# Kernel optimization log

Hardware: AMD Instinct MI355X
Metric: run time of the kernel (lower is better)

## Reference

```python
import jax, jax.numpy as jnp
import numpy as np

B, S, T, H, VS, VE = 32, 128, 128, 512, 8000, 8000


def _lstm_scan(x_proj, W_hh, bias, h0, c0):
    # x_proj: [L, B, 4H] precomputed input projections; gate order i,f,g,o (PyTorch)
    def step(carry, xp):
        h, c = carry
        gates = xp + h @ W_hh.T + bias  # [B, 4H]
        i, f, g, o = jnp.split(gates, 4, axis=-1)
        c = jax.nn.sigmoid(f) * c + jax.nn.sigmoid(i) * jnp.tanh(g)
        h = jax.nn.sigmoid(o) * jnp.tanh(c)
        return (h, c), h
    (h, c), hs = jax.lax.scan(step, (h0, c0), x_proj)
    return hs, h, c


def setup_inputs() -> dict:
    key = jax.random.key(0)
    ks = jax.random.split(key, 16)
    sc_h = 1.0 / np.sqrt(H)
    u = lambda k, shape: jax.random.uniform(k, shape, jnp.float32, -sc_h, sc_h)
    return {
        "input_batch": jax.random.randint(ks[0], (B, S), 0, VS),
        "output_batch": jax.random.randint(ks[1], (B, T), 0, VE),
        "Wa": u(ks[2], (H, H)), "ba": u(ks[3], (H,)),
        "W1": u(ks[4], (H, 2 * H)), "b1": u(ks[5], (H,)),
        "W2": u(ks[6], (VE, H)), "b2": u(ks[7], (VE,)),
        "We_ih": u(ks[8], (4 * H, VS)), "We_hh": u(ks[9], (4 * H, H)),
        "be_ih": u(ks[10], (4 * H,)), "be_hh": u(ks[11], (4 * H,)),
        "Wd_ih": u(ks[12], (4 * H, VE)), "Wd_hh": u(ks[13], (4 * H, H)),
        "bd_ih": u(ks[14], (4 * H,)), "bd_hh": u(ks[15], (4 * H,)),
    }


def reference(input_batch, output_batch, Wa, ba, W1, b1, W2, b2,
              We_ih, We_hh, be_ih, be_hh, Wd_ih, Wd_hh, bd_ih, bd_hh):
    src = input_batch.T  # [S, B]
    tgt = output_batch.T  # [T, B]
    # one_hot(tok) @ W_ih.T  ==  W_ih.T[tok]  (gather instead of dense one-hot GEMM)
    enc_xp = jnp.take(We_ih.T, src, axis=0)  # [S, B, 4H]
    dec_xp = jnp.take(Wd_ih.T, tgt, axis=0)  # [T, B, 4H]
    h0 = jnp.zeros((B, H), jnp.float32)
    c0 = jnp.zeros((B, H), jnp.float32)
    enc_outputs, h, c = _lstm_scan(enc_xp, We_hh, be_ih + be_hh, h0, c0)  # [S,B,H]
    proj_enc = enc_outputs @ Wa.T + ba  # attn(enc_outputs): [S, B, H]
    dec_bias = bd_ih + bd_hh

    def dec_step(carry, xp):
        h, c = carry
        gates = xp + h @ Wd_hh.T + dec_bias
        i, f, g, o = jnp.split(gates, 4, axis=-1)
        c = jax.nn.sigmoid(f) * c + jax.nn.sigmoid(i) * jnp.tanh(g)
        h = jax.nn.sigmoid(o) * jnp.tanh(c)  # [B, H] == dec_output
        scores = jnp.einsum('sbh,bh->bs', proj_enc, h)  # [B, S]
        w = jax.nn.softmax(scores, axis=1)
        context = jnp.einsum('bs,sbh->bh', w, enc_outputs)  # [B, H]
        hid = jnp.tanh(jnp.concatenate([h, context], axis=1) @ W1.T + b1)
        logits = hid @ W2.T + b2  # [B, VE]
        return (h, c), logits

    _, model = jax.lax.scan(dec_step, (h, c), dec_xp)  # [T, B, VE]
    return jax.nn.softmax(model.transpose(1, 0, 2), axis=2)  # [B, T, VE]
```

## Files before the change

### kernel.cpp

```cpp
#include <hip/hip_runtime.h>
#include <hip/hip_cooperative_groups.h>

#define NB 32
#define NS 128
#define NT 128
#define NH 512
#define NVS 8000
#define NVE 8000

typedef float fx4 __attribute__((ext_vector_type(4)));
typedef short bf16x8 __attribute__((ext_vector_type(8)));
typedef float f32x4 __attribute__((ext_vector_type(4)));

__device__ __forceinline__ float sigm(float x) { return 1.0f / (1.0f + expf(-x)); }

__device__ __forceinline__ fx4 load_cg(const float* p) {
  fx4 v;
  asm volatile("global_load_dwordx4 %0, %1, off sc0 sc1" : "=v"(v) : "v"(p));
  return v;
}
__device__ __forceinline__ void store_cg(float* p, fx4 v) {
  asm volatile("global_store_dwordx4 %0, %1, off sc0 sc1" :: "v"(p), "v"(v) : "memory");
}

__global__ __launch_bounds__(256) void scan_kernel(
    const int* __restrict__ in_tok, const int* __restrict__ out_tok,
    const float* __restrict__ We_ih, const float* __restrict__ We_hh,
    const float* __restrict__ be_ih, const float* __restrict__ be_hh,
    const float* __restrict__ Wd_ih, const float* __restrict__ Wd_hh,
    const float* __restrict__ bd_ih, const float* __restrict__ bd_hh,
    float* __restrict__ h_buf,
    float* __restrict__ enc_out,
    float* __restrict__ dec_h,
    int* __restrict__ flags)
{
  __shared__ float W_lds[16][520];
  __shared__ float h_lds[16 * 516];
  __shared__ float gbuf[16][16];
  __shared__ float c_buf[4][16];
  __shared__ float hstage[16][4];

  const int tid = threadIdx.x;
  const int g   = blockIdx.x;
  const int bg  = g & 1;
  const int mg  = g >> 1;
  const int r   = tid >> 4;
  const int bl  = tid & 15;
  const int b   = bg * 16 + bl;
  const int q   = r >> 2;
  const int i   = r & 3;
  const int j   = q * NH + mg * 4 + i;

  const float bias_e = be_ih[j] + be_hh[j];
  const float bias_d = bd_ih[j] + bd_hh[j];
  const float* Wcol_e = We_ih + (size_t)j * NVS;
  const float* Wcol_d = Wd_ih + (size_t)j * NVE;

  if (tid < 64) c_buf[tid >> 4][tid & 15] = 0.0f;

  {
    const float* Wg = We_hh;
    for (int u = tid; u < 2048; u += 256) {
      const int rr = u >> 7;
      const int k4 = (u & 127) << 2;
      const int jj = (rr >> 2) * NH + mg * 4 + (rr & 3);
      *(float4*)&W_lds[rr][k4] = *(const float4*)(Wg + (size_t)jj * NH + k4);
    }
  }
  __syncthreads();

  for (int s = 0; s < NS + NT; ++s) {
    const bool enc = (s < NS);
    if (s == NS) {
      const float* Wg = Wd_hh;
      for (int u = tid; u < 2048; u += 256) {
        const int rr = u >> 7;
        const int k4 = (u & 127) << 2;
        const int jj = (rr >> 2) * NH + mg * 4 + (rr & 3);
        *(float4*)&W_lds[rr][k4] = *(const float4*)(Wg + (size_t)jj * NH + k4);
      }
      __syncthreads();
    }
    const int st  = enc ? s : s - NS;
    const int tok = enc ? in_tok[b * NS + st] : out_tok[b * NT + st];
    const float xp = enc ? Wcol_e[tok] : Wcol_d[tok];
    const float bias = enc ? bias_e : bias_d;
    const float* Wrow = &W_lds[r][0];

    float acc = 0.0f;
    if (s > 0) {
      if (tid < 128) {
        const int idx = (tid << 1) | bg;
        while (__hip_atomic_load(&flags[idx], __ATOMIC_RELAXED,
                                 __HIP_MEMORY_SCOPE_AGENT) < s)
          __builtin_amdgcn_s_sleep(1);
      }
      __syncthreads();
      const float* hsrc = h_buf + ((s - 1) & 1) * (NB * NH) + bg * 16 * NH;
      fx4 tmp[8];
      #pragma unroll
      for (int it = 0; it < 8; ++it)
        tmp[it] = load_cg(hsrc + ((tid + (it << 8)) << 2));
      asm volatile("s_waitcnt vmcnt(0)" ::: "memory");
      __builtin_amdgcn_sched_barrier(0);
      #pragma unroll
      for (int it = 0; it < 8; ++it) {
        const int u = tid + (it << 8);
        const int bb = u >> 7;
        const int kk = (u & 127) << 2;
        *(fx4*)&h_lds[bb * 516 + kk] = tmp[it];
      }
      __syncthreads();
      const float* hrow = &h_lds[bl * 516];
      #pragma unroll 8
      for (int k = 0; k < NH; k += 4) {
        const float4 hv = *(const float4*)(hrow + k);
        const float4 wv = *(const float4*)(Wrow + k);
        acc += hv.x * wv.x + hv.y * wv.y + hv.z * wv.z + hv.w * wv.w;
      }
    }
    gbuf[r][bl] = acc + xp + bias;
    __syncthreads();

    if (tid < 64) {
      const int ii = tid >> 4;
      const int bb = tid & 15;
      const float gi = gbuf[ii][bb];
      const float gf = gbuf[4 + ii][bb];
      const float gg = gbuf[8 + ii][bb];
      const float go = gbuf[12 + ii][bb];
      const float co = c_buf[ii][bb];
      const float cn = sigm(gf) * co + sigm(gi) * tanhf(gg);
      const float hn = sigm(go) * tanhf(cn);
      c_buf[ii][bb] = cn;
      hstage[bb][ii] = hn;
    }
    __syncthreads();
    if (tid < 16) {
      const fx4 hv = *(const fx4*)&hstage[tid][0];
      const int bglob = bg * 16 + tid;
      store_cg(h_buf + (s & 1) * (NB * NH) + bglob * NH + mg * 4, hv);
      float* dst = enc ? (enc_out + ((size_t)st * NB + bglob) * NH + mg * 4)
                       : (dec_h  + ((size_t)st * NB + bglob) * NH + mg * 4);
      *(fx4*)dst = hv;
    }
    asm volatile("s_waitcnt vmcnt(0)" ::: "memory");
    __syncthreads();
    if (tid == 0)
      __hip_atomic_store(&flags[g], s + 1, __ATOMIC_RELAXED,
                         __HIP_MEMORY_SCOPE_AGENT);
  }
}

template<int TRANSB, int CSWAP, int ACT>
__global__ __launch_bounds__(256) void gemm64(
    const float* __restrict__ A, const float* __restrict__ Bm,
    float* __restrict__ C, const float* __restrict__ bias,
    const float* __restrict__ A2, int ksplit,
    int M, int N, int K, int lda, int ldb, int ldc,
    long batchA, long batchB, long batchC)
{
  __shared__ float As[16][68];
  __shared__ float Bs[16][68];
  const int z = blockIdx.z;
  A += (long)z * batchA;
  if (A2 != nullptr) A2 += (long)z * batchA;
  Bm += (long)z * batchB;
  C  += (long)z * batchC;
  const int m0 = blockIdx.y << 6;
  const int n0 = blockIdx.x << 6;
  const int tid = threadIdx.x;
  const int tx = tid & 15;
  const int ty = tid >> 4;
  float acc[4][4] = {};

  for (int k0 = 0; k0 < K; k0 += 16) {
    {
      const int mrow = tid >> 2;
      const int kcq = (tid & 3) << 2;
      const float* base = A;
      int keff = k0;
      if (A2 != nullptr && k0 >= ksplit) { base = A2; keff = k0 - ksplit; }
      const float4 v = *(const float4*)(base + (long)(m0 + mrow) * lda + keff + kcq);
      As[kcq + 0][mrow] = v.x; As[kcq + 1][mrow] = v.y;
      As[kcq + 2][mrow] = v.z; As[kcq + 3][mrow] = v.w;
    }
    if (TRANSB == 0) {
      const int nrow = tid >> 2;
      const int kcq = (tid & 3) << 2;
      const float4 v = *(const float4*)(Bm + (long)(n0 + nrow) * ldb + k0 + kcq);
      Bs[kcq + 0][nrow] = v.x; Bs[kcq + 1][nrow] = v.y;
      Bs[kcq + 2][nrow] = v.z; Bs[kcq + 3][nrow] = v.w;
    } else {
      const int krow = tid >> 4;
      const int nc = (tid & 15) << 2;
      const float4 v = *(const float4*)(Bm + (long)(k0 + krow) * ldb + n0 + nc);
      *(float4*)&Bs[krow][nc] = v;
    }
    __syncthreads();
    #pragma unroll
    for (int kk = 0; kk < 16; ++kk) {
      const float4 a4 = *(const float4*)&As[kk][ty << 2];
      const float4 b4 = *(const float4*)&Bs[kk][tx << 2];
      const float a[4]  = {a4.x, a4.y, a4.z, a4.w};
      const float bv[4] = {b4.x, b4.y, b4.z, b4.w};
      #pragma unroll
      for (int ii = 0; ii < 4; ++ii)
        #pragma unroll
        for (int jj = 0; jj < 4; ++jj)
          acc[ii][jj] = fmaf(a[ii], bv[jj], acc[ii][jj]);
    }
    __syncthreads();
  }

  const int n = n0 + (tx << 2);
  float4 bb4 = {0.f, 0.f, 0.f, 0.f};
  if (bias) { bb4.x = bias[n]; bb4.y = bias[n + 1]; bb4.z = bias[n + 2]; bb4.w = bias[n + 3]; }
  #pragma unroll
  for (int ii = 0; ii < 4; ++ii) {
    const int mrow = m0 + (ty << 2) + ii;
    float4 o;
    o.x = acc[ii][0] + bb4.x; o.y = acc[ii][1] + bb4.y;
    o.z = acc[ii][2] + bb4.z; o.w = acc[ii][3] + bb4.w;
    if (ACT == 1) { o.x = tanhf(o.x); o.y = tanhf(o.y); o.z = tanhf(o.z); o.w = tanhf(o.w); }
    long orow = mrow;
    if (CSWAP) orow = (long)(mrow & (NB - 1)) * NT + (mrow >> 5);
    *(float4*)(C + orow * (long)ldc + n) = o;
  }
}

__global__ __launch_bounds__(256) void split_bf16(
    const float* __restrict__ x, unsigned short* __restrict__ hi,
    unsigned short* __restrict__ lo, int n4)
{
  for (int i = blockIdx.x * 256 + threadIdx.x; i < n4; i += gridDim.x * 256) {
    const float4 v = ((const float4*)x)[i];
    float f[4] = {v.x, v.y, v.z, v.w};
    unsigned short hh[4], ll[4];
    #pragma unroll
    for (int jj = 0; jj < 4; ++jj) {
      const unsigned int u = __float_as_uint(f[jj]);
      const unsigned int r = (u + 0x7FFFu + ((u >> 16) & 1u)) >> 16;
      hh[jj] = (unsigned short)r;
      const float hf = __uint_as_float(r << 16);
      const float lf = f[jj] - hf;
      const unsigned int u2 = __float_as_uint(lf);
      const unsigned int r2 = (u2 + 0x7FFFu + ((u2 >> 16) & 1u)) >> 16;
      ll[jj] = (unsigned short)r2;
    }
    ushort4 hv, lv;
    hv.x = hh[0]; hv.y = hh[1]; hv.z = hh[2]; hv.w = hh[3];
    lv.x = ll[0]; lv.y = ll[1]; lv.z = ll[2]; lv.w = ll[3];
    ((ushort4*)hi)[i] = hv;
    ((ushort4*)lo)[i] = lv;
  }
}

template<int ACT, int OUT>
__global__ __launch_bounds__(256) void gemm_mfma(
    const unsigned short* __restrict__ Ahi, const unsigned short* __restrict__ Alo,
    const unsigned short* __restrict__ A2hi, const unsigned short* __restrict__ A2lo,
    int ksplit,
    const unsigned short* __restrict__ Bhi, const unsigned short* __restrict__ Blo,
    float* __restrict__ C, unsigned short* __restrict__ outHi,
    unsigned short* __restrict__ outLo, const float* __restrict__ bias,
    int K, int lda, int ldb, int ldc)
{
  __shared__ unsigned short BsH[64 * 32];
  __shared__ unsigned short BsL[64 * 32];
  const int tid  = threadIdx.x;
  const int wid  = tid >> 6;
  const int lane = tid & 63;
  const int l15  = lane & 15;
  const int kg   = lane >> 4;
  const int m0   = (blockIdx.y << 7) + (wid << 5);
  const int n0   = blockIdx.x << 6;
  const int srow = tid >> 2;
  const int scol = (tid & 3) << 3;

  f32x4 acc[2][4];
  #pragma unroll
  for (int fm = 0; fm < 2; ++fm)
    #pragma unroll
    for (int fn = 0; fn < 4; ++fn)
      acc[fm][fn] = (f32x4){0.f, 0.f, 0.f, 0.f};

  for (int k0 = 0; k0 < K; k0 += 32) {
    __syncthreads();
    *(bf16x8*)&BsH[srow * 32 + scol] =
        *(const bf16x8*)(Bhi + (size_t)(n0 + srow) * ldb + k0 + scol);
    *(bf16x8*)&BsL[srow * 32 + scol] =
        *(const bf16x8*)(Blo + (size_t)(n0 + srow) * ldb + k0 + scol);
    __syncthreads();

    const unsigned short* baseH = Ahi;
    const unsigned short* baseL = Alo;
    int keff = k0;
    if (A2hi != nullptr && k0 >= ksplit) {
      baseH = A2hi; baseL = A2lo; keff = k0 - ksplit;
    }
    bf16x8 ah[2], al[2];
    #pragma unroll
    for (int fm = 0; fm < 2; ++fm) {
      const size_t ro = (size_t)(m0 + (fm << 4) + l15) * lda + keff + (kg << 3);
      ah[fm] = *(const bf16x8*)(baseH + ro);
      al[fm] = *(const bf16x8*)(baseL + ro);
    }
    #pragma unroll
    for (int fm = 0; fm < 2; ++fm) {
      #pragma unroll
      for (int fn = 0; fn < 4; ++fn) {
        const bf16x8 bh  = *(const bf16x8*)&BsH[(((fn << 4) + l15) << 5) + (kg << 3)];
        const bf16x8 blv = *(const bf16x8*)&BsL[(((fn << 4) + l15) << 5) + (kg << 3)];
        acc[fm][fn] = __builtin_amdgcn_mfma_f32_16x16x32_bf16(
            ah[fm], bh, acc[fm][fn], 0, 0, 0);
        acc[fm][fn] = __builtin_amdgcn_mfma_f32_16x16x32_bf16(
            ah[fm], blv, acc[fm][fn], 0, 0, 0);
        acc[fm][fn] = __builtin_amdgcn_mfma_f32_16x16x32_bf16(
            al[fm], bh, acc[fm][fn], 0, 0, 0);
      }
    }
  }

  #pragma unroll
  for (int fm = 0; fm < 2; ++fm) {
    #pragma unroll
    for (int fn = 0; fn < 4; ++fn) {
      const int n = n0 + (fn << 4) + l15;
      const float bb = bias ? bias[n] : 0.0f;
      #pragma unroll
      for (int rg = 0; rg < 4; ++rg) {
        const int m = m0 + (fm << 4) + (kg << 2) + rg;
        float v = acc[fm][fn][rg] + bb;
        if (ACT == 1) v = tanhf(v);
        if (OUT == 2) {
          const unsigned int u = __float_as_uint(v);
          const unsigned int rv = (u + 0x7FFFu + ((u >> 16) & 1u)) >> 16;
          const float hf = __uint_as_float(rv << 16);
          const float lf = v - hf;
          const unsigned int u2 = __float_as_uint(lf);
          const unsigned int rl = (u2 + 0x7FFFu + ((u2 >> 16) & 1u)) >> 16;
          outHi[(size_t)m * ldc + n] = (unsigned short)rv;
          outLo[(size_t)m * ldc + n] = (unsigned short)rl;
        } else {
          C[(size_t)m * ldc + n] = v;
        }
      }
    }
  }
}

__global__ __launch_bounds__(256) void gemm_mfma_logits(
    const unsigned short* __restrict__ Ahi, const unsigned short* __restrict__ Alo,
    const unsigned short* __restrict__ Bhi, const unsigned short* __restrict__ Blo,
    float* __restrict__ C, const float* __restrict__ bias)
{
  __shared__ unsigned short BsH[64 * 32];
  __shared__ unsigned short BsL[64 * 32];
  const int tid  = threadIdx.x;
  const int wid  = tid >> 6;
  const int lane = tid & 63;
  const int l15  = lane & 15;
  const int kg   = lane >> 4;
  const int m0   = (blockIdx.y << 7) + (wid << 5);
  const int n0   = blockIdx.x << 6;

  const size_t aoff = (size_t)(m0 + l15) * NH + (kg << 3);
  const int srow = tid >> 2;
  const int scol = (tid & 3) << 3;

  f32x4 acc[2][4];
  #pragma unroll
  for (int fm = 0; fm < 2; ++fm)
    #pragma unroll
    for (int fn = 0; fn < 4; ++fn)
      acc[fm][fn] = (f32x4){0.f, 0.f, 0.f, 0.f};

  for (int k0 = 0; k0 < NH; k0 += 32) {
    __syncthreads();
    *(bf16x8*)&BsH[srow * 32 + scol] =
        *(const bf16x8*)(Bhi + (size_t)(n0 + srow) * NH + k0 + scol);
    *(bf16x8*)&BsL[srow * 32 + scol] =
        *(const bf16x8*)(Blo + (size_t)(n0 + srow) * NH + k0 + scol);
    __syncthreads();

    bf16x8 ah[2], al[2];
    #pragma unroll
    for (int fm = 0; fm < 2; ++fm) {
      ah[fm] = *(const bf16x8*)(Ahi + aoff + (size_t)(fm << 4) * NH + k0);
      al[fm] = *(const bf16x8*)(Alo + aoff + (size_t)(fm << 4) * NH + k0);
    }
    #pragma unroll
    for (int fm = 0; fm < 2; ++fm) {
      #pragma unroll
      for (int fn = 0; fn < 4; ++fn) {
        const bf16x8 bh  = *(const bf16x8*)&BsH[(((fn << 4) + l15) << 5) + (kg << 3)];
        const bf16x8 blv = *(const bf16x8*)&BsL[(((fn << 4) + l15) << 5) + (kg << 3)];
        acc[fm][fn] = __builtin_amdgcn_mfma_f32_16x16x32_bf16(
            ah[fm], bh, acc[fm][fn], 0, 0, 0);
        acc[fm][fn] = __builtin_amdgcn_mfma_f32_16x16x32_bf16(
            ah[fm], blv, acc[fm][fn], 0, 0, 0);
        acc[fm][fn] = __builtin_amdgcn_mfma_f32_16x16x32_bf16(
            al[fm], bh, acc[fm][fn], 0, 0, 0);
      }
    }
  }

  #pragma unroll
  for (int fm = 0; fm < 2; ++fm) {
    #pragma unroll
    for (int fn = 0; fn < 4; ++fn) {
      const int n = n0 + (fn << 4) + l15;
      const float bb = bias[n];
      #pragma unroll
      for (int rg = 0; rg < 4; ++rg) {
        const int m = m0 + (fm << 4) + (kg << 2) + rg;
        const long orow = (long)(m & (NB - 1)) * NT + (m >> 5);
        C[orow * NVE + n] = acc[fm][fn][rg] + bb;
      }
    }
  }
}

__global__ __launch_bounds__(128) void softmax_s(float* __restrict__ sc) {
  const long row = blockIdx.x;
  float* p = sc + row * NS;
  const float x = p[threadIdx.x];
  float mx = x;
  for (int o = 32; o; o >>= 1) mx = fmaxf(mx, __shfl_xor(mx, o));
  __shared__ float r0[2], r1[2];
  const int w = threadIdx.x >> 6;
  if ((threadIdx.x & 63) == 0) r0[w] = mx;
  __syncthreads();
  mx = fmaxf(r0[0], r0[1]);
  const float e = expf(x - mx);
  float sum = e;
  for (int o = 32; o; o >>= 1) sum += __shfl_xor(sum, o);
  if ((threadIdx.x & 63) == 0) r1[w] = sum;
  __syncthreads();
  sum = r1[0] + r1[1];
  p[threadIdx.x] = e / sum;
}

__global__ __launch_bounds__(256) void softmax_v(float* __restrict__ out) {
  const long row = blockIdx.x;
  float* p = out + row * NVE;
  float v[32];
  float mx = -1e30f;
  #pragma unroll
  for (int it = 0; it < 32; ++it) {
    const int idx = (it << 8) + threadIdx.x;
    v[it] = (idx < NVE) ? p[idx] : -1e30f;
    mx = fmaxf(mx, v[it]);
  }
  for (int o = 32; o; o >>= 1) mx = fmaxf(mx, __shfl_xor(mx, o));
  __shared__ float red[4], red2[4];
  const int w = threadIdx.x >> 6;
  if ((threadIdx.x & 63) == 0) red[w] = mx;
  __syncthreads();
  mx = fmaxf(fmaxf(red[0], red[1]), fmaxf(red[2], red[3]));
  float sum = 0.0f;
  #pragma unroll
  for (int it = 0; it < 32; ++it) {
    const int idx = (it << 8) + threadIdx.x;
    if (idx < NVE) { v[it] = expf(v[it] - mx); sum += v[it]; }
  }
  for (int o = 32; o; o >>= 1) sum += __shfl_xor(sum, o);
  if ((threadIdx.x & 63) == 0) red2[w] = sum;
  __syncthreads();
  sum = red2[0] + red2[1] + red2[2] + red2[3];
  const float inv = 1.0f / sum;
  #pragma unroll
  for (int it = 0; it < 32; ++it) {
    const int idx = (it << 8) + threadIdx.x;
    if (idx < NVE) p[idx] = v[it] * inv;
  }
}

extern "C" void kernel_launch(void* const* d_in, const int* in_sizes, int n_in,
                              void* d_out, int out_size, void* d_ws, size_t ws_size,
                              hipStream_t stream) {
  const int*   in_tok = (const int*)d_in[0];
  const int*   out_tok = (const int*)d_in[1];
  const float* Wa    = (const float*)d_in[2];
  const float* ba    = (const float*)d_in[3];
  const float* W1    = (const float*)d_in[4];
  const float* b1    = (const float*)d_in[5];
  const float* W2    = (const float*)d_in[6];
  const float* b2    = (const float*)d_in[7];
  const float* We_ih = (const float*)d_in[8];
  const float* We_hh = (const float*)d_in[9];
  const float* be_ih = (const float*)d_in[10];
  const float* be_hh = (const float*)d_in[11];
  const float* Wd_ih = (const float*)d_in[12];
  const float* Wd_hh = (const float*)d_in[13];
  const float* bd_ih = (const float*)d_in[14];
  const float* bd_hh = (const float*)d_in[15];

  float* ws      = (float*)d_ws;
  float* h_buf   = ws;
  float* enc_out = ws + 32768;
  float* dec_h   = ws + 2129920;
  float* proj    = ws + 4227072;
  float* scores  = ws + 6324224;
  float* ctx     = ws + 6848512;
  int*   flags   = (int*)(ws + 11042816);
  float* out     = (float*)d_out;

  unsigned short* eo_hi  = (unsigned short*)(ws + 8945664);
  unsigned short* eo_lo  = (unsigned short*)(ws + 8945664 + 1048576);
  unsigned short* wa_hi  = (unsigned short*)(ws + 6324224);
  unsigned short* wa_lo  = (unsigned short*)(ws + 6324224 + 131072);
  unsigned short* w1_hi  = (unsigned short*)(ws + 4227072);
  unsigned short* w1_lo  = (unsigned short*)(ws + 4227072 + 262144);
  unsigned short* dh_hi  = (unsigned short*)(ws + 32768);
  unsigned short* dh_lo  = (unsigned short*)(ws + 32768 + 1048576);
  unsigned short* cx_hi  = (unsigned short*)(ws + 2129920);
  unsigned short* cx_lo  = (unsigned short*)(ws + 2129920 + 1048576);
  unsigned short* hid_hi = (unsigned short*)(ws + 6848512);
  unsigned short* hid_lo = (unsigned short*)(ws + 6848512 + 1048576);
  unsigned short* w2_hi  = (unsigned short*)(ws + 8945664);
  unsigned short* w2_lo  = (unsigned short*)(ws + 32768);

  (void)hipMemsetAsync((void*)flags, 0, 256 * sizeof(int), stream);

  {
    void* args[14];
    args[0] = (void*)&in_tok; args[1] = (void*)&out_tok;
    args[2] = (void*)&We_ih;  args[3] = (void*)&We_hh;
    args[4] = (void*)&be_ih;  args[5] = (void*)&be_hh;
    args[6] = (void*)&Wd_ih;  args[7] = (void*)&Wd_hh;
    args[8] = (void*)&bd_ih;  args[9] = (void*)&bd_hh;
    args[10] = (void*)&h_buf; args[11] = (void*)&enc_out; args[12] = (void*)&dec_h;
    args[13] = (void*)&flags;
    (void)hipLaunchCooperativeKernel((void*)scan_kernel, dim3(256), dim3(256), args, 0, stream);
  }

  split_bf16<<<dim3(2048), 256, 0, stream>>>(enc_out, eo_hi, eo_lo, 524288);
  split_bf16<<<dim3(512), 256, 0, stream>>>(Wa, wa_hi, wa_lo, 65536);

  gemm_mfma<0, 0><<<dim3(8, 32), 256, 0, stream>>>(
      eo_hi, eo_lo, nullptr, nullptr, 1 << 30,
      wa_hi, wa_lo, proj, nullptr, nullptr, ba,
      512, 512, 512, 512);

  gemm64<0,0,0><<<dim3(2,2,NB), 256, 0, stream>>>(
      dec_h, proj, scores, nullptr, nullptr, 1 << 30,
      NT, NS, NH, NB * NH, NB * NH, NB * NS,
      (long)NH, (long)NH, (long)NS);

  softmax_s<<<dim3(NT * NB), 128, 0, stream>>>(scores);

  split_bf16<<<dim3(1024), 256, 0, stream>>>(W1, w1_hi, w1_lo, 131072);

  gemm64<1,0,0><<<dim3(8,2,NB), 256, 0, stream>>>(
      scores, enc_out, ctx, nullptr, nullptr, 1 << 30,
      NT, NH, NS, NB * NS, NB * NH, NB * NH,
      (long)NS, (long)NH, (long)NH);

  split_bf16<<<dim3(2048), 256, 0, stream>>>(dec_h, dh_hi, dh_lo, 524288);
  split_bf16<<<dim3(2048), 256, 0, stream>>>(ctx, cx_hi, cx_lo, 524288);

  gemm_mfma<1, 2><<<dim3(8, 32), 256, 0, stream>>>(
      dh_hi, dh_lo, cx_hi, cx_lo, 512,
      w1_hi, w1_lo, nullptr, hid_hi, hid_lo, b1,
      1024, 512, 1024, 512);

  split_bf16<<<dim3(2048), 256, 0, stream>>>(W2, w2_hi, w2_lo, 1024000);

  gemm_mfma_logits<<<dim3(125, 32), 256, 0, stream>>>(
      hid_hi, hid_lo, w2_hi, w2_lo, out, b2);

  softmax_v<<<dim3(NB * NT), 256, 0, stream>>>(out);
}
```

Measured before the change: 1.951 ms.

## Split LSTM scan across 512 blocks of 128 threads with 2 hidden units each

Result: slower. 2.116 ms (+8.5%).

```diff
diff --git a/kernel.cpp b/kernel.cpp
--- a/kernel.cpp
+++ b/kernel.cpp
@@ -9,6 +9,7 @@
 #define NVE 8000
 
 typedef float fx4 __attribute__((ext_vector_type(4)));
+typedef float fx2 __attribute__((ext_vector_type(2)));
 typedef short bf16x8 __attribute__((ext_vector_type(8)));
 typedef float f32x4 __attribute__((ext_vector_type(4)));
 
@@ -19,11 +20,11 @@
   asm volatile("global_load_dwordx4 %0, %1, off sc0 sc1" : "=v"(v) : "v"(p));
   return v;
 }
-__device__ __forceinline__ void store_cg(float* p, fx4 v) {
-  asm volatile("global_store_dwordx4 %0, %1, off sc0 sc1" :: "v"(p), "v"(v) : "memory");
-}
-
-__global__ __launch_bounds__(256) void scan_kernel(
+__device__ __forceinline__ void store_cg8(float* p, fx2 v) {
+  asm volatile("global_store_dwordx2 %0, %1, off sc0 sc1" :: "v"(p), "v"(v) : "memory");
+}
+
+__global__ __launch_bounds__(128) void scan_kernel(
     const int* __restrict__ in_tok, const int* __restrict__ out_tok,
     const float* __restrict__ We_ih, const float* __restrict__ We_hh,
     const float* __restrict__ be_ih, const float* __restrict__ be_hh,
@@ -34,36 +35,39 @@
     float* __restrict__ dec_h,
     int* __restrict__ flags)
 {
-  __shared__ float W_lds[16][520];
+  __shared__ float W_lds[8][520];
   __shared__ float h_lds[16 * 516];
-  __shared__ float gbuf[16][16];
-  __shared__ float c_buf[4][16];
-  __shared__ float hstage[16][4];
+  __shared__ float gbuf[8][16];
+  __shared__ float c_buf[2][16];
+  __shared__ float hstage[16][2];
 
   const int tid = threadIdx.x;
   const int g   = blockIdx.x;
   const int bg  = g & 1;
-  const int mg  = g >> 1;
+  const int mg2 = g >> 1;
   const int r   = tid >> 4;
   const int bl  = tid & 15;
   const int b   = bg * 16 + bl;
-  const int q   = r >> 2;
-  const int i   = r & 3;
-  const int j   = q * NH + mg * 4 + i;
+  const int q   = r >> 1;
+  const int i   = r & 1;
+  const int j   = q * NH + mg2 * 2 + i;
+
+  const int* f0 = flags + ((tid << 1) | bg);
+  const int* f1 = flags + (((tid + 128) << 1) | bg);
 
   const float bias_e = be_ih[j] + be_hh[j];
   const float bias_d = bd_ih[j] + bd_hh[j];
   const float* Wcol_e = We_ih + (size_t)j * NVS;
   const float* Wcol_d = Wd_ih + (size_t)j * NVE;
 
-  if (tid < 64) c_buf[tid >> 4][tid & 15] = 0.0f;
+  if (tid < 32) c_buf[tid >> 4][tid & 15] = 0.0f;
 
   {
     const float* Wg = We_hh;
-    for (int u = tid; u < 2048; u += 256) {
+    for (int u = tid; u < 1024; u += 128) {
       const int rr = u >> 7;
       const int k4 = (u & 127) << 2;
-      const int jj = (rr >> 2) * NH + mg * 4 + (rr & 3);
+      const int jj = (rr >> 1) * NH + mg2 * 2 + (rr & 1);
       *(float4*)&W_lds[rr][k4] = *(const float4*)(Wg + (size_t)jj * NH + k4);
     }
   }
@@ -73,10 +77,10 @@
     const bool enc = (s < NS);
     if (s == NS) {
       const float* Wg = Wd_hh;
-      for (int u = tid; u < 2048; u += 256) {
+      for (int u = tid; u < 1024; u += 128) {
         const int rr = u >> 7;
         const int k4 = (u & 127) << 2;
-        const int jj = (rr >> 2) * NH + mg * 4 + (rr & 3);
+        const int jj = (rr >> 1) * NH + mg2 * 2 + (rr & 1);
         *(float4*)&W_lds[rr][k4] = *(const float4*)(Wg + (size_t)jj * NH + k4);
       }
       __syncthreads();
@@ -89,23 +93,22 @@
 
     float acc = 0.0f;
     if (s > 0) {
-      if (tid < 128) {
-        const int idx = (tid << 1) | bg;
-        while (__hip_atomic_load(&flags[idx], __ATOMIC_RELAXED,
-                                 __HIP_MEMORY_SCOPE_AGENT) < s)
-          __builtin_amdgcn_s_sleep(1);
-      }
+      while (__hip_atomic_load(f0, __ATOMIC_RELAXED,
+                               __HIP_MEMORY_SCOPE_AGENT) < s ||
+             __hip_atomic_load(f1, __ATOMIC_RELAXED,
+                               __HIP_MEMORY_SCOPE_AGENT) < s)
+        __builtin_amdgcn_s_sleep(1);
       __syncthreads();
       const float* hsrc = h_buf + ((s - 1) & 1) * (NB * NH) + bg * 16 * NH;
-      fx4 tmp[8];
-      #pragma unroll
-      for (int it = 0; it < 8; ++it)
-        tmp[it] = load_cg(hsrc + ((tid + (it << 8)) << 2));
+      fx4 tmp[16];
+      #pragma unroll
+      for (int it = 0; it < 16; ++it)
+        tmp[it] = load_cg(hsrc + ((tid + (it << 7)) << 2));
       asm volatile("s_waitcnt vmcnt(0)" ::: "memory");
       __builtin_amdgcn_sched_barrier(0);
       #pragma unroll
-      for (int it = 0; it < 8; ++it) {
-        const int u = tid + (it << 8);
+      for (int it = 0; it < 16; ++it) {
+        const int u = tid + (it << 7);
         const int bb = u >> 7;
         const int kk = (u & 127) << 2;
         *(fx4*)&h_lds[bb * 516 + kk] = tmp[it];
@@ -122,13 +125,13 @@
     gbuf[r][bl] = acc + xp + bias;
     __syncthreads();
 
-    if (tid < 64) {
+    if (tid < 32) {
       const int ii = tid >> 4;
       const int bb = tid & 15;
       const float gi = gbuf[ii][bb];
-      const float gf = gbuf[4 + ii][bb];
-      const float gg = gbuf[8 + ii][bb];
-      const float go = gbuf[12 + ii][bb];
+      const float gf = gbuf[2 + ii][bb];
+      const float gg = gbuf[4 + ii][bb];
+      const float go = gbuf[6 + ii][bb];
       const float co = c_buf[ii][bb];
       const float cn = sigm(gf) * co + sigm(gi) * tanhf(gg);
       const float hn = sigm(go) * tanhf(cn);
@@ -137,12 +140,12 @@
     }
     __syncthreads();
     if (tid < 16) {
-      const fx4 hv = *(const fx4*)&hstage[tid][0];
+      const fx2 hv = *(const fx2*)&hstage[tid][0];
       const int bglob = bg * 16 + tid;
-      store_cg(h_buf + (s & 1) * (NB * NH) + bglob * NH + mg * 4, hv);
-      float* dst = enc ? (enc_out + ((size_t)st * NB + bglob) * NH + mg * 4)
-                       : (dec_h  + ((size_t)st * NB + bglob) * NH + mg * 4);
-      *(fx4*)dst = hv;
+      store_cg8(h_buf + (s & 1) * (NB * NH) + bglob * NH + mg2 * 2, hv);
+      float* dst = enc ? (enc_out + ((size_t)st * NB + bglob) * NH + mg2 * 2)
+                       : (dec_h  + ((size_t)st * NB + bglob) * NH + mg2 * 2);
+      *(fx2*)dst = hv;
     }
     asm volatile("s_waitcnt vmcnt(0)" ::: "memory");
     __syncthreads();
@@ -522,7 +525,7 @@
   unsigned short* w2_hi  = (unsigned short*)(ws + 8945664);
   unsigned short* w2_lo  = (unsigned short*)(ws + 32768);
 
-  (void)hipMemsetAsync((void*)flags, 0, 256 * sizeof(int), stream);
+  (void)hipMemsetAsync((void*)flags, 0, 512 * sizeof(int), stream);
 
   {
     void* args[14];
@@ -533,7 +536,7 @@
     args[8] = (void*)&bd_ih;  args[9] = (void*)&bd_hh;
     args[10] = (void*)&h_buf; args[11] = (void*)&enc_out; args[12] = (void*)&dec_h;
     args[13] = (void*)&flags;
-    (void)hipLaunchCooperativeKernel((void*)scan_kernel, dim3(256), dim3(256), args, 0, stream);
+    (void)hipLaunchCooperativeKernel((void*)scan_kernel, dim3(512), dim3(128), args, 0, stream);
   }
 
   split_bf16<<<dim3(2048), 256, 0, stream>>>(enc_out, eo_hi, eo_lo, 524288);
```
